# Optimization experiments

Hardware: AMD Instinct MI355X
Metric: run time of the kernel (lower is better)

## Reference

```python
import jax, jax.numpy as jnp
import numpy as np

B, T, E, UNITS, VOCAB, NCLS = 128, 512, 256, 256, 50257, 2

def setup_inputs() -> dict:
    key = jax.random.key(0)
    ks = jax.random.split(key, 7)
    s = 0.05
    return {
        "sentence": jax.random.randint(ks[0], (B, T), 0, VOCAB, dtype=jnp.int32),
        "emb_table": jax.random.normal(ks[1], (VOCAB, E), jnp.float32) * s,
        "W": jax.random.normal(ks[2], (1, UNITS, E), jnp.float32) * s,
        "U": jax.random.normal(ks[3], (1, UNITS, UNITS), jnp.float32) * s,
        "W1": jax.random.normal(ks[4], (UNITS, 32), jnp.float32) * s,
        "b1": jnp.zeros((32,), jnp.float32),
        "W2": jax.random.normal(ks[5], (32, NCLS), jnp.float32) * s,
        "b2": jnp.zeros((NCLS,), jnp.float32),
    }

def reference(sentence, emb_table, W, U, W1, b1, W2, b2):
    # Embedding lookup: [B, T, E]
    emb = emb_table[sentence]
    # Precompute input projection for all timesteps in one batched GEMM:
    # x @ W[0].T for every t -> [T, B, units]
    xW = jnp.einsum('bte,ue->tbu', emb, W[0])
    Ut = U[0].T  # [units, units]

    def step(h, xw_t):
        h_new = jnp.tanh(xw_t + h @ Ut)
        return h_new, None

    h0 = jnp.zeros((sentence.shape[0], W.shape[1]), emb.dtype)
    h_final, _ = jax.lax.scan(step, h0, xW)

    # Classification head (dropout is identity at inference)
    hidden = jax.nn.relu(h_final @ W1 + b1)
    logits = hidden @ W2 + b2
    return jax.nn.softmax(logits, axis=-1)
```

## Files before the change

### kernel.cpp

```cpp
#include <hip/hip_runtime.h>
#include <hip/hip_bf16.h>
#include <stdint.h>

#define TT 512
#define NB 128
#define EM 256
#define UN 256

typedef short bf16x8 __attribute__((ext_vector_type(8)));
typedef float floatx4 __attribute__((ext_vector_type(4)));
typedef _Float16 half8 __attribute__((ext_vector_type(8)));
typedef int v8i __attribute__((ext_vector_type(8)));

#define SCALE_A 0x7D7D7D7DU
#define SCALE_B 0x7B7B7B7BU

#define BAR() asm volatile("s_waitcnt lgkmcnt(0)\n\ts_barrier" ::: "memory")

__device__ inline unsigned short f2bf(float f) {
    union { float f; uint32_t u; } v; v.f = f;
    uint32_t r = v.u + 0x7fffu + ((v.u >> 16) & 1u);
    return (unsigned short)(r >> 16);
}
__device__ inline float bf2f(unsigned short b) {
    union { uint32_t u; float f; } v; v.u = ((uint32_t)b) << 16;
    return v.f;
}
__device__ inline unsigned char f2fp8(float f) {
    int pk = __builtin_amdgcn_cvt_pk_fp8_f32(f, f, 0, false);
    return (unsigned char)(pk & 0xff);
}
__device__ inline float fp8d(unsigned char b) {
    int s = b >> 7, e = (b >> 3) & 15, m = b & 7;
    float v = e ? ldexpf((float)(8 + m), e - 10) : ldexpf((float)m, -9);
    return s ? -v : v;
}

__global__ void k_pack(const float* __restrict__ W, const float* __restrict__ U,
                       unsigned short* __restrict__ wfrag, unsigned char* __restrict__ ufrag8) {
    int bid = blockIdx.x;
    if (bid < 32) {
        int idx = bid * 256 + threadIdx.x;
        int lane = idx & 63;
        int tile = idx >> 6;
        int nt = tile & 15, kt = tile >> 4;
        int u  = nt * 16 + (lane & 15);
        int e0 = kt * 32 + (lane >> 4) * 8;
        unsigned short* dst = wfrag + (size_t)idx * 8;
        #pragma unroll
        for (int j = 0; j < 8; j++) dst[j] = f2bf(W[u * EM + e0 + j]);
    } else {
        int idx = (bid - 32) * 256 + threadIdx.x;
        int jg   = idx & 3;
        int lane = (idx >> 2) & 63;
        int tile = idx >> 8;
        int nt = tile & 15, kh = tile >> 4;
        int u  = nt * 16 + (lane & 15);
        int k0 = kh * 128 + (lane >> 4) * 32 + jg * 8;
        unsigned char* dst = ufrag8 + ((size_t)tile * 64 + lane) * 32 + jg * 8;
        #pragma unroll
        for (int j = 0; j < 8; j++) dst[j] = f2fp8(16.f * U[u * UN + k0 + j]);
    }
}

__global__ __launch_bounds__(256, 2) void k_gemm(
    const int* __restrict__ sent, const float* __restrict__ emb,
    const unsigned short* __restrict__ wfrag, unsigned short* __restrict__ xw)
{
    __shared__ unsigned short gt[64][264];
    int w    = threadIdx.x >> 6;
    int lane = threadIdx.x & 63;
    int m  = lane & 15;
    int kg = lane >> 4;
    int row = blockIdx.x * 64 + w * 16 + m;
    int tok = sent[row];
    const float* arow = emb + (size_t)tok * EM;

    bf16x8 a[8];
    #pragma unroll
    for (int kt = 0; kt < 8; kt++) {
        const float* p = arow + kt * 32 + kg * 8;
        float4 f0 = *(const float4*)p;
        float4 f1 = *(const float4*)(p + 4);
        bf16x8 t;
        t[0] = (short)f2bf(f0.x); t[1] = (short)f2bf(f0.y);
        t[2] = (short)f2bf(f0.z); t[3] = (short)f2bf(f0.w);
        t[4] = (short)f2bf(f1.x); t[5] = (short)f2bf(f1.y);
        t[6] = (short)f2bf(f1.z); t[7] = (short)f2bf(f1.w);
        a[kt] = t;
    }

    floatx4 acc[16];
    #pragma unroll
    for (int nt = 0; nt < 16; nt++) acc[nt] = floatx4{0.f, 0.f, 0.f, 0.f};

    #pragma unroll
    for (int kt = 0; kt < 8; kt++) {
        #pragma unroll
        for (int nt = 0; nt < 16; nt++) {
            bf16x8 bfr = *(const bf16x8*)(wfrag + ((size_t)(kt * 16 + nt) * 64 + lane) * 8);
            acc[nt] = __builtin_amdgcn_mfma_f32_16x16x32_bf16(a[kt], bfr, acc[nt], 0, 0, 0);
        }
    }

    int rloc = w * 16 + kg * 4;
    #pragma unroll
    for (int nt = 0; nt < 16; nt++) {
        #pragma unroll
        for (int r = 0; r < 4; r++) {
            gt[rloc + r][nt * 16 + m] = f2bf(acc[nt][r]);
        }
    }
    __syncthreads();

    int rowbase = blockIdx.x * 64;
    #pragma unroll
    for (int r2 = 0; r2 < 16; r2++) {
        int rr = w * 16 + r2;
        uint2 v = *(const uint2*)&gt[rr][lane * 4];
        *(uint2*)(xw + (size_t)(rowbase + rr) * UN + lane * 4) = v;
    }
}

__global__ __launch_bounds__(256, 1) void k_rnn(
    const unsigned char* __restrict__ ufrag8, const unsigned short* __restrict__ xw,
    const float* __restrict__ W1, const float* __restrict__ b1,
    const float* __restrict__ W2, const float* __restrict__ b2,
    float* __restrict__ out)
{
    __shared__ __align__(16) unsigned char hb8[2][256];
    __shared__ __align__(16) unsigned short xstage[64 * 256];
    __shared__ float hid[32];
    const int t    = threadIdx.x;
    const int lane = t & 63;
    const int w    = t >> 6;
    const int kg   = lane >> 4;
    const int b    = blockIdx.x;

    v8i ufr8[4][2];
    #pragma unroll
    for (int q = 0; q < 4; q++) {
        #pragma unroll
        for (int kh = 0; kh < 2; kh++) {
            const uint4* p = (const uint4*)(ufrag8 + ((size_t)(kh * 16 + 4 * w + q) * 64 + lane) * 32);
            union { uint4 u4[2]; v8i v; } cvt;
            cvt.u4[0] = p[0]; cvt.u4[1] = p[1];
            ufr8[q][kh] = cvt.v;
        }
    }

    const unsigned short* xwb = xw + (size_t)b * TT * UN;
    const int roff = w * 512 + lane * 8;

    uint4 xr[8];
    #pragma unroll
    for (int p = 0; p < 8; p++) xr[p] = *(const uint4*)(xwb + roff + p * 2048);
    #pragma unroll
    for (int p = 0; p < 8; p++) *(uint4*)&xstage[roff + p * 2048] = xr[p];

    hb8[0][t] = 0; hb8[1][t] = 0;
    __syncthreads();

    int cur = 0;
    const float c3 = -0.33333334f, c5 = 0.13333334f, c7 = -0.05396825f, c9 = 0.02186949f;
    const floatx4 zero4 = {0.f, 0.f, 0.f, 0.f};
    const int sel = lane >> 4;

    for (int s = 0; s < TT; s++) {
        const int ls = s & 63;
        unsigned short xv = xstage[ls * 256 + t];

        const unsigned char* hc = hb8[cur];
        union { uint4 u4[2]; v8i v; } A0, A1;
        A0.u4[0] = *(const uint4*)(hc + kg * 32);
        A0.u4[1] = *(const uint4*)(hc + kg * 32 + 16);
        A1.u4[0] = *(const uint4*)(hc + 128 + kg * 32);
        A1.u4[1] = *(const uint4*)(hc + 128 + kg * 32 + 16);

        float z[4];
        #pragma unroll
        for (int q = 0; q < 4; q++) {
            floatx4 acc = zero4;
            acc = __builtin_amdgcn_mfma_scale_f32_16x16x128_f8f6f4(
                      A0.v, ufr8[q][0], acc, 0, 0, 0, SCALE_A, 0, SCALE_B);
            acc = __builtin_amdgcn_mfma_scale_f32_16x16x128_f8f6f4(
                      A1.v, ufr8[q][1], acc, 0, 0, 0, SCALE_A, 0, SCALE_B);
            z[q] = acc[0];
        }

        float zz = (sel == 0) ? z[0] : (sel == 1) ? z[1] : (sel == 2) ? z[2] : z[3];
        zz += bf2f(xv);

        float hn;
        if (__builtin_expect(fabsf(zz) > 0.75f, 0)) {
            float e = __expf(2.f * zz);
            hn = 1.f - 2.f * __builtin_amdgcn_rcpf(e + 1.f);
        } else {
            float x2f = zz * zz;
            float p = fmaf(x2f, c9, c7);
            p = fmaf(x2f, p, c5);
            p = fmaf(x2f, p, c3);
            hn = fmaf(zz * x2f, p, zz);
        }

        hb8[cur ^ 1][t] = f2fp8(4.f * hn);

        if (ls == 60 && s + 68 <= TT) {
            const unsigned short* cb = xwb + (size_t)(s + 4) * UN;
            #pragma unroll
            for (int p = 0; p < 8; p++) xr[p] = *(const uint4*)(cb + roff + p * 2048);
        }
        if (ls == 63 && s + 65 <= TT) {
            BAR();
            #pragma unroll
            for (int p = 0; p < 8; p++) *(uint4*)&xstage[roff + p * 2048] = xr[p];
        }
        BAR();
        cur ^= 1;
    }

    if (t < 32) {
        float a = b1[t];
        for (int k = 0; k < 256; k++) a += 0.25f * fp8d(hb8[cur][k]) * W1[k * 32 + t];
        hid[t] = fmaxf(a, 0.f);
    }
    __syncthreads();
    if (t == 0) {
        float l0 = b2[0], l1 = b2[1];
        #pragma unroll
        for (int i = 0; i < 32; i++) {
            float hv = hid[i];
            l0 += hv * W2[2 * i];
            l1 += hv * W2[2 * i + 1];
        }
        float mx2 = fmaxf(l0, l1);
        float e0 = __expf(l0 - mx2), e1 = __expf(l1 - mx2);
        float inv = 1.f / (e0 + e1);
        out[2 * b]     = e0 * inv;
        out[2 * b + 1] = e1 * inv;
    }
}

extern "C" void kernel_launch(void* const* d_in, const int* in_sizes, int n_in,
                              void* d_out, int out_size, void* d_ws, size_t ws_size,
                              hipStream_t stream) {
    const int*   sent = (const int*)d_in[0];
    const float* emb  = (const float*)d_in[1];
    const float* W    = (const float*)d_in[2];
    const float* U    = (const float*)d_in[3];
    const float* W1   = (const float*)d_in[4];
    const float* b1   = (const float*)d_in[5];
    const float* W2   = (const float*)d_in[6];
    const float* b2   = (const float*)d_in[7];
    float* out = (float*)d_out;

    unsigned short* xw     = (unsigned short*)d_ws;
    unsigned short* wfrag  = (unsigned short*)((char*)d_ws + (size_t)NB * TT * UN * 2);
    unsigned char*  ufrag8 = (unsigned char*)((char*)d_ws + (size_t)NB * TT * UN * 2 + (size_t)UN * EM * 2);

    k_pack<<<64, 256, 0, stream>>>(W, U, wfrag, ufrag8);
    k_gemm<<<(NB * TT) / 64, 256, 0, stream>>>(sent, emb, wfrag, xw);
    k_rnn<<<NB, 256, 0, stream>>>(ufrag8, xw, W1, b1, W2, b2, out);
}
```

Measured before the change: 333.4 us.

## Split recurrent matvec across 8 waves with 2 MFMA tiles each

The per-batch RNN kernel now runs 512 threads (8 waves) per block instead of 256. Each wave computes two 16-column output tiles instead of four, which halves the serial MFMA chain per timestep. Half of each wave's lanes write the new hidden state. The cost is more threads joining every per-step barrier, plus redundant lanes that compute values which are then discarded.

```diff
diff --git a/kernel.cpp b/kernel.cpp
--- a/kernel.cpp
+++ b/kernel.cpp
@@ -9,7 +9,6 @@
 
 typedef short bf16x8 __attribute__((ext_vector_type(8)));
 typedef float floatx4 __attribute__((ext_vector_type(4)));
-typedef _Float16 half8 __attribute__((ext_vector_type(8)));
 typedef int v8i __attribute__((ext_vector_type(8)));
 
 #define SCALE_A 0x7D7D7D7DU
@@ -122,7 +121,7 @@
     }
 }
 
-__global__ __launch_bounds__(256, 1) void k_rnn(
+__global__ __launch_bounds__(512, 1) void k_rnn(
     const unsigned char* __restrict__ ufrag8, const unsigned short* __restrict__ xw,
     const float* __restrict__ W1, const float* __restrict__ b1,
     const float* __restrict__ W2, const float* __restrict__ b2,
@@ -137,38 +136,39 @@
     const int kg   = lane >> 4;
     const int b    = blockIdx.x;
 
-    v8i ufr8[4][2];
-    #pragma unroll
-    for (int q = 0; q < 4; q++) {
+    v8i ufr8[2][2];
+    #pragma unroll
+    for (int dt = 0; dt < 2; dt++) {
         #pragma unroll
         for (int kh = 0; kh < 2; kh++) {
-            const uint4* p = (const uint4*)(ufrag8 + ((size_t)(kh * 16 + 4 * w + q) * 64 + lane) * 32);
+            const uint4* p = (const uint4*)(ufrag8 + ((size_t)(kh * 16 + 2 * w + dt) * 64 + lane) * 32);
             union { uint4 u4[2]; v8i v; } cvt;
             cvt.u4[0] = p[0]; cvt.u4[1] = p[1];
-            ufr8[q][kh] = cvt.v;
+            ufr8[dt][kh] = cvt.v;
         }
     }
 
     const unsigned short* xwb = xw + (size_t)b * TT * UN;
-    const int roff = w * 512 + lane * 8;
-
-    uint4 xr[8];
-    #pragma unroll
-    for (int p = 0; p < 8; p++) xr[p] = *(const uint4*)(xwb + roff + p * 2048);
-    #pragma unroll
-    for (int p = 0; p < 8; p++) *(uint4*)&xstage[roff + p * 2048] = xr[p];
-
-    hb8[0][t] = 0; hb8[1][t] = 0;
+    const int roff = t * 8;
+
+    uint4 xr[4];
+    #pragma unroll
+    for (int p = 0; p < 4; p++) xr[p] = *(const uint4*)(xwb + roff + p * 4096);
+    #pragma unroll
+    for (int p = 0; p < 4; p++) *(uint4*)&xstage[roff + p * 4096] = xr[p];
+
+    if (t < 256) { hb8[0][t] = 0; hb8[1][t] = 0; }
     __syncthreads();
 
     int cur = 0;
     const float c3 = -0.33333334f, c5 = 0.13333334f, c7 = -0.05396825f, c9 = 0.02186949f;
     const floatx4 zero4 = {0.f, 0.f, 0.f, 0.f};
-    const int sel = lane >> 4;
+    const int myu   = 32 * w + (lane & 31);
+    const int dtsel = (lane >> 4) & 1;
 
     for (int s = 0; s < TT; s++) {
         const int ls = s & 63;
-        unsigned short xv = xstage[ls * 256 + t];
+        float xf = bf2f(xstage[ls * 256 + myu]);
 
         const unsigned char* hc = hb8[cur];
         union { uint4 u4[2]; v8i v; } A0, A1;
@@ -177,19 +177,17 @@
         A1.u4[0] = *(const uint4*)(hc + 128 + kg * 32);
         A1.u4[1] = *(const uint4*)(hc + 128 + kg * 32 + 16);
 
-        float z[4];
-        #pragma unroll
-        for (int q = 0; q < 4; q++) {
-            floatx4 acc = zero4;
+        float z[2];
+        #pragma unroll
+        for (int dt = 0; dt < 2; dt++) {
+            floatx4 acc = __builtin_amdgcn_mfma_scale_f32_16x16x128_f8f6f4(
+                              A0.v, ufr8[dt][0], zero4, 0, 0, 0, SCALE_A, 0, SCALE_B);
             acc = __builtin_amdgcn_mfma_scale_f32_16x16x128_f8f6f4(
-                      A0.v, ufr8[q][0], acc, 0, 0, 0, SCALE_A, 0, SCALE_B);
-            acc = __builtin_amdgcn_mfma_scale_f32_16x16x128_f8f6f4(
-                      A1.v, ufr8[q][1], acc, 0, 0, 0, SCALE_A, 0, SCALE_B);
-            z[q] = acc[0];
-        }
-
-        float zz = (sel == 0) ? z[0] : (sel == 1) ? z[1] : (sel == 2) ? z[2] : z[3];
-        zz += bf2f(xv);
+                              A1.v, ufr8[dt][1], acc, 0, 0, 0, SCALE_A, 0, SCALE_B);
+            z[dt] = acc[0];
+        }
+
+        float zz = (dtsel ? z[1] : z[0]) + xf;
 
         float hn;
         if (__builtin_expect(fabsf(zz) > 0.75f, 0)) {
@@ -203,17 +201,17 @@
             hn = fmaf(zz * x2f, p, zz);
         }
 
-        hb8[cur ^ 1][t] = f2fp8(4.f * hn);
+        if (lane < 32) hb8[cur ^ 1][myu] = f2fp8(4.f * hn);
 
         if (ls == 60 && s + 68 <= TT) {
             const unsigned short* cb = xwb + (size_t)(s + 4) * UN;
             #pragma unroll
-            for (int p = 0; p < 8; p++) xr[p] = *(const uint4*)(cb + roff + p * 2048);
+            for (int p = 0; p < 4; p++) xr[p] = *(const uint4*)(cb + roff + p * 4096);
         }
         if (ls == 63 && s + 65 <= TT) {
             BAR();
             #pragma unroll
-            for (int p = 0; p < 8; p++) *(uint4*)&xstage[roff + p * 2048] = xr[p];
+            for (int p = 0; p < 4; p++) *(uint4*)&xstage[roff + p * 4096] = xr[p];
         }
         BAR();
         cur ^= 1;
@@ -260,5 +258,5 @@
 
     k_pack<<<64, 256, 0, stream>>>(W, U, wfrag, ufrag8);
     k_gemm<<<(NB * TT) / 64, 256, 0, stream>>>(sent, emb, wfrag, xw);
-    k_rnn<<<NB, 256, 0, stream>>>(ufrag8, xw, W1, b1, W2, b2, out);
-}
+    k_rnn<<<NB, 512, 0, stream>>>(ufrag8, xw, W1, b1, W2, b2, out);
+}
```

Result: no change. 335.1 us (+0.5%).

## Switch input projection GEMM and xW intermediate from bf16 to fp8

Applied to the files above, without the earlier changes.

The embedding×W GEMM now quantizes both operands to fp8 and runs on scaled fp8 MFMA (16x16x128) in place of bf16 MFMA. The xW intermediate is stored as fp8, which halves its global write and read traffic and the LDS staging size in the recurrent kernel. The xW values are decoded with a hardware cvt builtin when available. This adds extra quantization error to the input projection.

```diff
diff --git a/kernel.cpp b/kernel.cpp
--- a/kernel.cpp
+++ b/kernel.cpp
@@ -7,13 +7,11 @@
 #define EM 256
 #define UN 256
 
-typedef short bf16x8 __attribute__((ext_vector_type(8)));
 typedef float floatx4 __attribute__((ext_vector_type(4)));
-typedef _Float16 half8 __attribute__((ext_vector_type(8)));
 typedef int v8i __attribute__((ext_vector_type(8)));
 
+#define SCALE_Q 0x7B7B7B7BU
 #define SCALE_A 0x7D7D7D7DU
-#define SCALE_B 0x7B7B7B7BU
 
 #define BAR() asm volatile("s_waitcnt lgkmcnt(0)\n\ts_barrier" ::: "memory")
 
@@ -22,52 +20,50 @@
     uint32_t r = v.u + 0x7fffu + ((v.u >> 16) & 1u);
     return (unsigned short)(r >> 16);
 }
-__device__ inline float bf2f(unsigned short b) {
-    union { uint32_t u; float f; } v; v.u = ((uint32_t)b) << 16;
-    return v.f;
-}
 __device__ inline unsigned char f2fp8(float f) {
     int pk = __builtin_amdgcn_cvt_pk_fp8_f32(f, f, 0, false);
     return (unsigned char)(pk & 0xff);
 }
-__device__ inline float fp8d(unsigned char b) {
+__device__ inline float fp8dec(uint32_t word, int sel) {
+#if defined(__has_builtin)
+#if __has_builtin(__builtin_amdgcn_cvt_f32_fp8)
+    return __builtin_amdgcn_cvt_f32_fp8(word >> (8 * sel), 0);
+#else
+    unsigned char b = (word >> (8 * sel)) & 0xff;
     int s = b >> 7, e = (b >> 3) & 15, m = b & 7;
     float v = e ? ldexpf((float)(8 + m), e - 10) : ldexpf((float)m, -9);
     return s ? -v : v;
+#endif
+#else
+    unsigned char b = (word >> (8 * sel)) & 0xff;
+    int s = b >> 7, e = (b >> 3) & 15, m = b & 7;
+    float v = e ? ldexpf((float)(8 + m), e - 10) : ldexpf((float)m, -9);
+    return s ? -v : v;
+#endif
 }
 
 __global__ void k_pack(const float* __restrict__ W, const float* __restrict__ U,
-                       unsigned short* __restrict__ wfrag, unsigned char* __restrict__ ufrag8) {
+                       unsigned char* __restrict__ wfrag8, unsigned char* __restrict__ ufrag8) {
     int bid = blockIdx.x;
-    if (bid < 32) {
-        int idx = bid * 256 + threadIdx.x;
-        int lane = idx & 63;
-        int tile = idx >> 6;
-        int nt = tile & 15, kt = tile >> 4;
-        int u  = nt * 16 + (lane & 15);
-        int e0 = kt * 32 + (lane >> 4) * 8;
-        unsigned short* dst = wfrag + (size_t)idx * 8;
-        #pragma unroll
-        for (int j = 0; j < 8; j++) dst[j] = f2bf(W[u * EM + e0 + j]);
-    } else {
-        int idx = (bid - 32) * 256 + threadIdx.x;
-        int jg   = idx & 3;
-        int lane = (idx >> 2) & 63;
-        int tile = idx >> 8;
-        int nt = tile & 15, kh = tile >> 4;
-        int u  = nt * 16 + (lane & 15);
-        int k0 = kh * 128 + (lane >> 4) * 32 + jg * 8;
-        unsigned char* dst = ufrag8 + ((size_t)tile * 64 + lane) * 32 + jg * 8;
-        #pragma unroll
-        for (int j = 0; j < 8; j++) dst[j] = f2fp8(16.f * U[u * UN + k0 + j]);
-    }
+    const float* src = (bid < 32) ? W : U;
+    unsigned char* dstbase = (bid < 32) ? wfrag8 : ufrag8;
+    int idx = (bid & 31) * 256 + threadIdx.x;
+    int jg   = idx & 3;
+    int lane = (idx >> 2) & 63;
+    int tile = idx >> 8;
+    int nt = tile & 15, kh = tile >> 4;
+    int u  = nt * 16 + (lane & 15);
+    int k0 = kh * 128 + (lane >> 4) * 32 + jg * 8;
+    unsigned char* dst = dstbase + ((size_t)tile * 64 + lane) * 32 + jg * 8;
+    #pragma unroll
+    for (int j = 0; j < 8; j++) dst[j] = f2fp8(16.f * src[u * EM + k0 + j]);
 }
 
 __global__ __launch_bounds__(256, 2) void k_gemm(
     const int* __restrict__ sent, const float* __restrict__ emb,
-    const unsigned short* __restrict__ wfrag, unsigned short* __restrict__ xw)
+    const unsigned char* __restrict__ wfrag8, unsigned char* __restrict__ xw8)
 {
-    __shared__ unsigned short gt[64][264];
+    __shared__ unsigned char gt[64][272];
     int w    = threadIdx.x >> 6;
     int lane = threadIdx.x & 63;
     int m  = lane & 15;
@@ -76,31 +72,33 @@
     int tok = sent[row];
     const float* arow = emb + (size_t)tok * EM;
 
-    bf16x8 a[8];
-    #pragma unroll
-    for (int kt = 0; kt < 8; kt++) {
-        const float* p = arow + kt * 32 + kg * 8;
-        float4 f0 = *(const float4*)p;
-        float4 f1 = *(const float4*)(p + 4);
-        bf16x8 t;
-        t[0] = (short)f2bf(f0.x); t[1] = (short)f2bf(f0.y);
-        t[2] = (short)f2bf(f0.z); t[3] = (short)f2bf(f0.w);
-        t[4] = (short)f2bf(f1.x); t[5] = (short)f2bf(f1.y);
-        t[6] = (short)f2bf(f1.z); t[7] = (short)f2bf(f1.w);
-        a[kt] = t;
-    }
-
+    union { uint32_t d[8]; v8i v; } A[2];
+    #pragma unroll
+    for (int kh = 0; kh < 2; kh++) {
+        const float* p = arow + kh * 128 + kg * 32;
+        #pragma unroll
+        for (int d = 0; d < 8; d++) {
+            float4 f = *(const float4*)(p + 4 * d);
+            int pk = __builtin_amdgcn_cvt_pk_fp8_f32(16.f * f.x, 16.f * f.y, 0, false);
+            pk     = __builtin_amdgcn_cvt_pk_fp8_f32(16.f * f.z, 16.f * f.w, pk, true);
+            A[kh].d[d] = (uint32_t)pk;
+        }
+    }
+
+    const floatx4 zero4 = {0.f, 0.f, 0.f, 0.f};
     floatx4 acc[16];
     #pragma unroll
-    for (int nt = 0; nt < 16; nt++) acc[nt] = floatx4{0.f, 0.f, 0.f, 0.f};
-
-    #pragma unroll
-    for (int kt = 0; kt < 8; kt++) {
-        #pragma unroll
-        for (int nt = 0; nt < 16; nt++) {
-            bf16x8 bfr = *(const bf16x8*)(wfrag + ((size_t)(kt * 16 + nt) * 64 + lane) * 8);
-            acc[nt] = __builtin_amdgcn_mfma_f32_16x16x32_bf16(a[kt], bfr, acc[nt], 0, 0, 0);
-        }
+    for (int nt = 0; nt < 16; nt++) {
+        union { uint4 u4[2]; v8i v; } B0, B1;
+        const uint4* p0 = (const uint4*)(wfrag8 + ((size_t)(0 * 16 + nt) * 64 + lane) * 32);
+        const uint4* p1 = (const uint4*)(wfrag8 + ((size_t)(1 * 16 + nt) * 64 + lane) * 32);
+        B0.u4[0] = p0[0]; B0.u4[1] = p0[1];
+        B1.u4[0] = p1[0]; B1.u4[1] = p1[1];
+        floatx4 a = __builtin_amdgcn_mfma_scale_f32_16x16x128_f8f6f4(
+                        A[0].v, B0.v, zero4, 0, 0, 0, SCALE_Q, 0, SCALE_Q);
+        a = __builtin_amdgcn_mfma_scale_f32_16x16x128_f8f6f4(
+                        A[1].v, B1.v, a, 0, 0, 0, SCALE_Q, 0, SCALE_Q);
+        acc[nt] = a;
     }
 
     int rloc = w * 16 + kg * 4;
@@ -108,7 +106,7 @@
     for (int nt = 0; nt < 16; nt++) {
         #pragma unroll
         for (int r = 0; r < 4; r++) {
-            gt[rloc + r][nt * 16 + m] = f2bf(acc[nt][r]);
+            gt[rloc + r][nt * 16 + m] = f2fp8(16.f * acc[nt][r]);
         }
     }
     __syncthreads();
@@ -117,19 +115,19 @@
     #pragma unroll
     for (int r2 = 0; r2 < 16; r2++) {
         int rr = w * 16 + r2;
-        uint2 v = *(const uint2*)&gt[rr][lane * 4];
-        *(uint2*)(xw + (size_t)(rowbase + rr) * UN + lane * 4) = v;
+        uint32_t v = *(const uint32_t*)&gt[rr][lane * 4];
+        *(uint32_t*)(xw8 + (size_t)(rowbase + rr) * UN + lane * 4) = v;
     }
 }
 
 __global__ __launch_bounds__(256, 1) void k_rnn(
-    const unsigned char* __restrict__ ufrag8, const unsigned short* __restrict__ xw,
+    const unsigned char* __restrict__ ufrag8, const unsigned char* __restrict__ xw8,
     const float* __restrict__ W1, const float* __restrict__ b1,
     const float* __restrict__ W2, const float* __restrict__ b2,
     float* __restrict__ out)
 {
     __shared__ __align__(16) unsigned char hb8[2][256];
-    __shared__ __align__(16) unsigned short xstage[64 * 256];
+    __shared__ __align__(16) unsigned char xstage[64 * 256];
     __shared__ float hid[32];
     const int t    = threadIdx.x;
     const int lane = t & 63;
@@ -149,14 +147,14 @@
         }
     }
 
-    const unsigned short* xwb = xw + (size_t)b * TT * UN;
-    const int roff = w * 512 + lane * 8;
-
-    uint4 xr[8];
-    #pragma unroll
-    for (int p = 0; p < 8; p++) xr[p] = *(const uint4*)(xwb + roff + p * 2048);
-    #pragma unroll
-    for (int p = 0; p < 8; p++) *(uint4*)&xstage[roff + p * 2048] = xr[p];
+    const unsigned char* xwb = xw8 + (size_t)b * TT * UN;
+    const int roff = t * 16;
+
+    uint4 xr[4];
+    #pragma unroll
+    for (int p = 0; p < 4; p++) xr[p] = *(const uint4*)(xwb + roff + p * 4096);
+    #pragma unroll
+    for (int p = 0; p < 4; p++) *(uint4*)&xstage[roff + p * 4096] = xr[p];
 
     hb8[0][t] = 0; hb8[1][t] = 0;
     __syncthreads();
@@ -168,7 +166,8 @@
 
     for (int s = 0; s < TT; s++) {
         const int ls = s & 63;
-        unsigned short xv = xstage[ls * 256 + t];
+        uint32_t xword = *(const uint32_t*)&xstage[ls * 256 + (t & ~3)];
+        float xf = fp8dec(xword, t & 3) * 0.0625f;
 
         const unsigned char* hc = hb8[cur];
         union { uint4 u4[2]; v8i v; } A0, A1;
@@ -180,16 +179,15 @@
         float z[4];
         #pragma unroll
         for (int q = 0; q < 4; q++) {
-            floatx4 acc = zero4;
+            floatx4 acc = __builtin_amdgcn_mfma_scale_f32_16x16x128_f8f6f4(
+                              A0.v, ufr8[q][0], zero4, 0, 0, 0, SCALE_A, 0, SCALE_Q);
             acc = __builtin_amdgcn_mfma_scale_f32_16x16x128_f8f6f4(
-                      A0.v, ufr8[q][0], acc, 0, 0, 0, SCALE_A, 0, SCALE_B);
-            acc = __builtin_amdgcn_mfma_scale_f32_16x16x128_f8f6f4(
-                      A1.v, ufr8[q][1], acc, 0, 0, 0, SCALE_A, 0, SCALE_B);
+                              A1.v, ufr8[q][1], acc, 0, 0, 0, SCALE_A, 0, SCALE_Q);
             z[q] = acc[0];
         }
 
         float zz = (sel == 0) ? z[0] : (sel == 1) ? z[1] : (sel == 2) ? z[2] : z[3];
-        zz += bf2f(xv);
+        zz += xf;
 
         float hn;
         if (__builtin_expect(fabsf(zz) > 0.75f, 0)) {
@@ -206,14 +204,14 @@
         hb8[cur ^ 1][t] = f2fp8(4.f * hn);
 
         if (ls == 60 && s + 68 <= TT) {
-            const unsigned short* cb = xwb + (size_t)(s + 4) * UN;
+            const unsigned char* cb = xwb + (size_t)(s + 4) * UN;
             #pragma unroll
-            for (int p = 0; p < 8; p++) xr[p] = *(const uint4*)(cb + roff + p * 2048);
+            for (int p = 0; p < 4; p++) xr[p] = *(const uint4*)(cb + roff + p * 4096);
         }
         if (ls == 63 && s + 65 <= TT) {
             BAR();
             #pragma unroll
-            for (int p = 0; p < 8; p++) *(uint4*)&xstage[roff + p * 2048] = xr[p];
+            for (int p = 0; p < 4; p++) *(uint4*)&xstage[roff + p * 4096] = xr[p];
         }
         BAR();
         cur ^= 1;
@@ -221,7 +219,10 @@
 
     if (t < 32) {
         float a = b1[t];
-        for (int k = 0; k < 256; k++) a += 0.25f * fp8d(hb8[cur][k]) * W1[k * 32 + t];
+        for (int k = 0; k < 256; k++) {
+            uint32_t wd = *(const uint32_t*)&hb8[cur][k & ~3];
+            a += 0.25f * fp8dec(wd, k & 3) * W1[k * 32 + t];
+        }
         hid[t] = fmaxf(a, 0.f);
     }
     __syncthreads();
@@ -254,11 +255,11 @@
     const float* b2   = (const float*)d_in[7];
     float* out = (float*)d_out;
 
-    unsigned short* xw     = (unsigned short*)d_ws;
-    unsigned short* wfrag  = (unsigned short*)((char*)d_ws + (size_t)NB * TT * UN * 2);
-    unsigned char*  ufrag8 = (unsigned char*)((char*)d_ws + (size_t)NB * TT * UN * 2 + (size_t)UN * EM * 2);
-
-    k_pack<<<64, 256, 0, stream>>>(W, U, wfrag, ufrag8);
-    k_gemm<<<(NB * TT) / 64, 256, 0, stream>>>(sent, emb, wfrag, xw);
-    k_rnn<<<NB, 256, 0, stream>>>(ufrag8, xw, W1, b1, W2, b2, out);
-}
+    unsigned char* xw8    = (unsigned char*)d_ws;
+    unsigned char* wfrag8 = (unsigned char*)d_ws + (size_t)NB * TT * UN;
+    unsigned char* ufrag8 = wfrag8 + (size_t)UN * EM;
+
+    k_pack<<<64, 256, 0, stream>>>(W, U, wfrag8, ufrag8);
+    k_gemm<<<(NB * TT) / 64, 256, 0, stream>>>(sent, emb, wfrag8, xw8);
+    k_rnn<<<NB, 256, 0, stream>>>(ufrag8, xw8, W1, b1, W2, b2, out);
+}
```

Result: faster. 302.5 us (-9.3%).
